# Kernel optimization log

Measured on AMD Instinct MI355X. Metric: run time of the kernel, lower is better.

## Reference

```python
import jax, jax.numpy as jnp
import numpy as np

N, H, S, R, T = 32768, 512, 8, 64, 12

def setup_inputs() -> dict:
    key = jax.random.key(0)
    ks = jax.random.split(key, 7)
    scale = 1.0 / np.sqrt(H)
    return {
        "encodings": jax.random.normal(ks[0], (N, H), dtype=jnp.float32),
        "domain_encs": jax.random.normal(ks[1], (S, H), dtype=jnp.float32),
        "Us": jax.random.normal(ks[2], (S, H, R), dtype=jnp.float32) * scale,
        "W1": jax.random.normal(ks[3], (S, H, H), dtype=jnp.float32) * scale,
        "b1": jax.random.normal(ks[4], (S, H), dtype=jnp.float32) * 0.01,
        "W2": jax.random.normal(ks[5], (S, H, T), dtype=jnp.float32) * scale,
        "b2": jax.random.normal(ks[6], (S, T), dtype=jnp.float32) * 0.01,
    }

def reference(encodings, domain_encs, Us, W1, b1, W2, b2):
    # Mahalanobis soft routing. Original computes (p-mu) @ (U U^T) @ (p-mu)^T
    # and takes sqrt(diag) -- algebraically identical to project-then-square-sum.
    diff = encodings[None, :, :] - domain_encs[:, None, :]        # [S, N, H]
    proj = jnp.einsum('snh,shr->snr', diff, Us)                   # [S, N, R]
    dist = jnp.sqrt(jnp.sum(proj * proj, axis=-1))                # [S, N]
    alphas = jax.nn.softmax(-dist, axis=0)                        # softmax over sources

    # Per-source classifier: Dropout(eval=identity) -> ReLU -> Linear(H,H)
    # -> Dropout -> ReLU -> Linear(H,T) -> Sigmoid
    h0 = jax.nn.relu(encodings)                                   # [N, H]
    h1 = jax.nn.relu(jnp.einsum('nh,shk->snk', h0, W1) + b1[:, None, :])  # [S, N, H]
    out = jax.nn.sigmoid(jnp.einsum('snk,skt->snt', h1, W2) + b2[:, None, :])  # [S, N, T]

    # Softmax-weighted combine of expert outputs
    return jnp.sum(alphas[:, :, None] * out, axis=0)              # [N, T]
```

## Files before the change

### kernel.cpp

```cpp
#include <hip/hip_runtime.h>
#include <hip/hip_bf16.h>

typedef unsigned short u16;
typedef __bf16 bf16x8 __attribute__((ext_vector_type(8)));
typedef float f32x4 __attribute__((ext_vector_type(4)));

#define NROWS 32768
#define H 512
#define NS 8
#define NR 64
#define NT 12

#define WS_W1T   0
#define WS_UCT   4194304
#define WS_W2T   4718592
#define WS_CVEC  4849664
#define WS_ALPH  4851712

union BFU { __bf16 h; u16 u; };
__device__ __forceinline__ u16 f2bf(float v) { BFU b; b.h = (__bf16)v; return b.u; }

__device__ __forceinline__ void gload16(const u16* g, u16* l) {
  __builtin_amdgcn_global_load_lds(
      (const __attribute__((address_space(1))) unsigned int*)g,
      (__attribute__((address_space(3))) unsigned int*)l, 16, 0, 0);
}

__device__ __forceinline__ void stage32(const u16* __restrict__ g, u16* l, int wave, int lane) {
#pragma unroll
  for (int i = 0; i < 8; i++) {
    int r = wave * 8 + i;
    gload16(g + (size_t)r * 512 + (size_t)((lane ^ (r & 7)) * 8), l + r * 512);
  }
}

__global__ __launch_bounds__(256) void transpose_cast(const float* __restrict__ in,
    u16* __restrict__ out, int Rr, int Cc, int Cpad) {
  __shared__ float tile[32][33];
  int b = blockIdx.z, r0 = blockIdx.x * 32, c0 = blockIdx.y * 32;
  int tx = threadIdx.x, ty = threadIdx.y;
#pragma unroll
  for (int i = 0; i < 4; i++) {
    int r = r0 + ty + i * 8, c = c0 + tx;
    float v = 0.f;
    if (r < Rr && c < Cc) v = in[((size_t)b * Rr + r) * Cc + c];
    tile[ty + i * 8][tx] = v;
  }
  __syncthreads();
#pragma unroll
  for (int i = 0; i < 4; i++) {
    int c = c0 + ty + i * 8, r = r0 + tx;
    if (c < Cpad && r < Rr) out[((size_t)b * Cpad + c) * Rr + r] = f2bf(tile[tx][ty + i * 8]);
  }
}

__global__ __launch_bounds__(64) void compute_c(const float* __restrict__ mu,
                                                const float* __restrict__ Us,
                                                float* __restrict__ cvec) {
  int s = blockIdx.x >> 6, r = blockIdx.x & 63, t = threadIdx.x;
  float acc = 0.f;
#pragma unroll
  for (int k = t; k < H; k += 64) acc += mu[s * H + k] * Us[((size_t)s * H + k) * NR + r];
#pragma unroll
  for (int m = 32; m; m >>= 1) acc += __shfl_xor(acc, m, 64);
  if (t == 0) cvec[blockIdx.x] = acc;
}

__global__ __launch_bounds__(256, 2) void routing(
    const float* __restrict__ enc, const u16* __restrict__ UcatT,
    const float* __restrict__ cvec, float* __restrict__ alphT) {
  __shared__ __align__(16) u16 Wst[2][32 * 512];
  __shared__ float distS[NS][64];

  const int tid = threadIdx.x;
  const int wave = tid >> 6, lane = tid & 63;
  const int lnm = lane & 15, lnq = lane >> 4;
  const int row0 = blockIdx.x * 64;

  bf16x8 afrag[16];
  {
    const float* rp = enc + (size_t)(row0 + wave * 16 + lnm) * H + lnq * 8;
#pragma unroll
    for (int ks = 0; ks < 16; ks++) {
      float4 x0 = *(const float4*)(rp + ks * 32);
      float4 x1 = *(const float4*)(rp + ks * 32 + 4);
      bf16x8 a;
      a[0] = (__bf16)x0.x; a[1] = (__bf16)x0.y; a[2] = (__bf16)x0.z; a[3] = (__bf16)x0.w;
      a[4] = (__bf16)x1.x; a[5] = (__bf16)x1.y; a[6] = (__bf16)x1.z; a[7] = (__bf16)x1.w;
      afrag[ks] = a;
    }
  }

  stage32(UcatT, Wst[0], wave, lane);
  float dsq[4] = {0.f, 0.f, 0.f, 0.f};
#pragma unroll 1
  for (int q = 0; q < 16; q++) {
    int s = q >> 1, half = q & 1;
    __syncthreads();
    if (q < 15) stage32(UcatT + (size_t)(q + 1) * 32 * 512, Wst[(q + 1) & 1], wave, lane);
    const u16* buf = Wst[q & 1];
    f32x4 acc[2] = {};
#pragma unroll
    for (int ks = 0; ks < 16; ks++) {
      int uu = ((ks * 4 + lnq) ^ (lnm & 7)) * 8;
      bf16x8 b0 = *(const bf16x8*)&buf[lnm * 512 + uu];
      bf16x8 b1v = *(const bf16x8*)&buf[(16 + lnm) * 512 + uu];
      acc[0] = __builtin_amdgcn_mfma_f32_16x16x32_bf16(afrag[ks], b0, acc[0], 0, 0, 0);
      acc[1] = __builtin_amdgcn_mfma_f32_16x16x32_bf16(afrag[ks], b1v, acc[1], 0, 0, 0);
    }
#pragma unroll
    for (int ct = 0; ct < 2; ct++) {
      float cv = cvec[s * 64 + half * 32 + ct * 16 + lnm];
#pragma unroll
      for (int g = 0; g < 4; g++) { float d = acc[ct][g] - cv; dsq[g] += d * d; }
    }
    if (half == 1) {
#pragma unroll
      for (int m = 1; m < 16; m <<= 1) {
#pragma unroll
        for (int g = 0; g < 4; g++) dsq[g] += __shfl_xor(dsq[g], m, 16);
      }
      if (lnm == 0) {
#pragma unroll
        for (int g = 0; g < 4; g++) distS[s][wave * 16 + lnq * 4 + g] = sqrtf(dsq[g]);
      }
#pragma unroll
      for (int g = 0; g < 4; g++) dsq[g] = 0.f;
    }
  }
  __syncthreads();
  if (tid < 64) {
    float dmin = distS[0][tid];
#pragma unroll
    for (int s = 1; s < NS; s++) dmin = fminf(dmin, distS[s][tid]);
    float den = 0.f, e[NS];
#pragma unroll
    for (int s = 0; s < NS; s++) { e[s] = __expf(dmin - distS[s][tid]); den += e[s]; }
    float inv = 1.f / den;
#pragma unroll
    for (int s = 0; s < NS; s++) alphT[(size_t)s * NROWS + row0 + tid] = e[s] * inv;
  }
}

__global__ __launch_bounds__(256, 2) void moe_main(
    const float* __restrict__ enc, const u16* __restrict__ W1T,
    const u16* __restrict__ W2T, const float* __restrict__ alphT,
    const float* __restrict__ b1g, const float* __restrict__ b2g,
    float* __restrict__ out) {
  __shared__ __align__(16) u16 Wst[2][32 * 512];
  __shared__ __align__(16) u16 h1c[128 * 48];
  __shared__ float alphS[4][128];

  const int tid = threadIdx.x;
  const int wave = tid >> 6, lane = tid & 63;
  const int lnm = lane & 15, lnq = lane >> 4;
  const int rb = blockIdx.x >> 1, sg = blockIdx.x & 1;
  const int row0 = rb * 128, sbase = sg * 4;

#pragma unroll
  for (int i = 0; i < 2; i++) {
    int u = tid + i * 256, j = u >> 7, r = u & 127;
    alphS[j][r] = alphT[(size_t)(sbase + j) * NROWS + row0 + r];
  }

  bf16x8 afrag[2][16];
#pragma unroll
  for (int t = 0; t < 2; t++) {
    const float* rp = enc + (size_t)(row0 + wave * 32 + t * 16 + lnm) * H + lnq * 8;
#pragma unroll
    for (int ks = 0; ks < 16; ks++) {
      float4 x0 = *(const float4*)(rp + ks * 32);
      float4 x1 = *(const float4*)(rp + ks * 32 + 4);
      bf16x8 a;
      a[0] = (__bf16)fmaxf(x0.x, 0.f); a[1] = (__bf16)fmaxf(x0.y, 0.f);
      a[2] = (__bf16)fmaxf(x0.z, 0.f); a[3] = (__bf16)fmaxf(x0.w, 0.f);
      a[4] = (__bf16)fmaxf(x1.x, 0.f); a[5] = (__bf16)fmaxf(x1.y, 0.f);
      a[6] = (__bf16)fmaxf(x1.z, 0.f); a[7] = (__bf16)fmaxf(x1.w, 0.f);
      afrag[t][ks] = a;
    }
  }

  stage32(W1T + (size_t)sbase * 512 * 512, Wst[0], wave, lane);
  f32x4 oacc[2] = {};
  float fin[2][4] = {};
#pragma unroll 1
  for (int q = 0; q < 64; q++) {
    const int j = q >> 4, ch = q & 15;
    const int s = sbase + j;
    __syncthreads();
    if (q < 63) {
      int q1 = q + 1;
      const u16* nb = W1T + ((size_t)(sbase + (q1 >> 4)) * 512 + (q1 & 15) * 32) * 512;
      stage32(nb, Wst[q1 & 1], wave, lane);
    }
    const u16* buf = Wst[q & 1];
    f32x4 acc[2][2] = {};
#pragma unroll
    for (int ks = 0; ks < 16; ks++) {
      int uu = ((ks * 4 + lnq) ^ (lnm & 7)) * 8;
      bf16x8 b0 = *(const bf16x8*)&buf[lnm * 512 + uu];
      bf16x8 b1v = *(const bf16x8*)&buf[(16 + lnm) * 512 + uu];
#pragma unroll
      for (int t = 0; t < 2; t++) {
        acc[t][0] = __builtin_amdgcn_mfma_f32_16x16x32_bf16(afrag[t][ks], b0, acc[t][0], 0, 0, 0);
        acc[t][1] = __builtin_amdgcn_mfma_f32_16x16x32_bf16(afrag[t][ks], b1v, acc[t][1], 0, 0, 0);
      }
    }
    float bb0 = b1g[s * H + ch * 32 + lnm];
    float bb1 = b1g[s * H + ch * 32 + 16 + lnm];
#pragma unroll
    for (int t = 0; t < 2; t++) {
#pragma unroll
      for (int g = 0; g < 4; g++) {
        int rr = wave * 32 + t * 16 + lnq * 4 + g;
        h1c[rr * 48 + lnm]      = f2bf(fmaxf(acc[t][0][g] + bb0, 0.f));
        h1c[rr * 48 + 16 + lnm] = f2bf(fmaxf(acc[t][1][g] + bb1, 0.f));
      }
    }
    bf16x8 bw = *(const bf16x8*)&W2T[((size_t)s * 16 + lnm) * 512 + ch * 32 + lnq * 8];
#pragma unroll
    for (int t = 0; t < 2; t++) {
      bf16x8 a2 = *(const bf16x8*)&h1c[(wave * 32 + t * 16 + lnm) * 48 + lnq * 8];
      oacc[t] = __builtin_amdgcn_mfma_f32_16x16x32_bf16(a2, bw, oacc[t], 0, 0, 0);
    }
    if (ch == 15) {
      float b2v = (lnm < NT) ? b2g[s * NT + lnm] : 0.f;
#pragma unroll
      for (int t = 0; t < 2; t++) {
#pragma unroll
        for (int g = 0; g < 4; g++) {
          float pre = oacc[t][g] + b2v;
          float sig = 1.f / (1.f + __expf(-pre));
          fin[t][g] += alphS[j][wave * 32 + t * 16 + lnq * 4 + g] * sig;
        }
        oacc[t] = (f32x4){0.f, 0.f, 0.f, 0.f};
      }
    }
  }
  if (lnm < NT) {
#pragma unroll
    for (int t = 0; t < 2; t++) {
#pragma unroll
      for (int g = 0; g < 4; g++) {
        int rg = row0 + wave * 32 + t * 16 + lnq * 4 + g;
        atomicAdd(&out[(size_t)rg * NT + lnm], fin[t][g]);
      }
    }
  }
}

extern "C" void kernel_launch(void* const* d_in, const int* in_sizes, int n_in,
                              void* d_out, int out_size, void* d_ws, size_t ws_size,
                              hipStream_t stream) {
  const float* enc = (const float*)d_in[0];
  const float* mu  = (const float*)d_in[1];
  const float* Us  = (const float*)d_in[2];
  const float* W1  = (const float*)d_in[3];
  const float* b1  = (const float*)d_in[4];
  const float* W2  = (const float*)d_in[5];
  const float* b2  = (const float*)d_in[6];
  float* out = (float*)d_out;
  char* ws = (char*)d_ws;
  u16* W1T    = (u16*)(ws + WS_W1T);
  u16* UcatT  = (u16*)(ws + WS_UCT);
  u16* W2T    = (u16*)(ws + WS_W2T);
  float* cvec = (float*)(ws + WS_CVEC);
  float* alphT = (float*)(ws + WS_ALPH);

  dim3 tb(32, 8, 1);
  transpose_cast<<<dim3(16, 16, 8), tb, 0, stream>>>(W1, W1T, 512, 512, 512);
  transpose_cast<<<dim3(16, 2, 8),  tb, 0, stream>>>(Us, UcatT, 512, 64, 64);
  transpose_cast<<<dim3(16, 1, 8),  tb, 0, stream>>>(W2, W2T, 512, 12, 16);
  compute_c<<<512, 64, 0, stream>>>(mu, Us, cvec);
  routing<<<512, 256, 0, stream>>>(enc, UcatT, cvec, alphT);
  hipMemsetAsync(out, 0, (size_t)out_size * sizeof(float), stream);
  moe_main<<<512, 256, 0, stream>>>(enc, W1T, W2T, alphT, b1, b2, out);
}
```

Baseline: 305.8 us.

## Retile moe_main to 256-row blocks with 32x32 MFMA and swapped operands

Rewrites the main MoE kernel so each block handles 256 rows and 2 sources instead of 128 rows and 4 sources. The first GEMM now uses 32x32x16 MFMAs with the weight tile as the A operand and the encodings held in registers as B. W1 chunks are staged in K-halves so the LDS buffers shrink, and occupancy is raised to 3 blocks per CU. The goal is more reuse of each staged weight tile across rows and fewer LDS reads per MFMA. In exchange, register pressure rises (64 bf16x8 fragments per thread) and the h1 tile is written transposed with packed stores.

```diff
diff --git a/kernel.cpp b/kernel.cpp
--- a/kernel.cpp
+++ b/kernel.cpp
@@ -4,6 +4,7 @@
 typedef unsigned short u16;
 typedef __bf16 bf16x8 __attribute__((ext_vector_type(8)));
 typedef float f32x4 __attribute__((ext_vector_type(4)));
+typedef float f32x16 __attribute__((ext_vector_type(16)));
 
 #define NROWS 32768
 #define H 512
@@ -26,14 +27,6 @@
       (__attribute__((address_space(3))) unsigned int*)l, 16, 0, 0);
 }
 
-__device__ __forceinline__ void stage32(const u16* __restrict__ g, u16* l, int wave, int lane) {
-#pragma unroll
-  for (int i = 0; i < 8; i++) {
-    int r = wave * 8 + i;
-    gload16(g + (size_t)r * 512 + (size_t)((lane ^ (r & 7)) * 8), l + r * 512);
-  }
-}
-
 __global__ __launch_bounds__(256) void transpose_cast(const float* __restrict__ in,
     u16* __restrict__ out, int Rr, int Cc, int Cpad) {
   __shared__ float tile[32][33];
@@ -64,6 +57,14 @@
 #pragma unroll
   for (int m = 32; m; m >>= 1) acc += __shfl_xor(acc, m, 64);
   if (t == 0) cvec[blockIdx.x] = acc;
+}
+
+__device__ __forceinline__ void stage32r(const u16* __restrict__ g, u16* l, int wave, int lane) {
+#pragma unroll
+  for (int i = 0; i < 8; i++) {
+    int r = wave * 8 + i;
+    gload16(g + (size_t)r * 512 + (size_t)((lane ^ (r & 7)) * 8), l + r * 512);
+  }
 }
 
 __global__ __launch_bounds__(256, 2) void routing(
@@ -91,13 +92,13 @@
     }
   }
 
-  stage32(UcatT, Wst[0], wave, lane);
+  stage32r(UcatT, Wst[0], wave, lane);
   float dsq[4] = {0.f, 0.f, 0.f, 0.f};
 #pragma unroll 1
   for (int q = 0; q < 16; q++) {
     int s = q >> 1, half = q & 1;
     __syncthreads();
-    if (q < 15) stage32(UcatT + (size_t)(q + 1) * 32 * 512, Wst[(q + 1) & 1], wave, lane);
+    if (q < 15) stage32r(UcatT + (size_t)(q + 1) * 32 * 512, Wst[(q + 1) & 1], wave, lane);
     const u16* buf = Wst[q & 1];
     f32x4 acc[2] = {};
 #pragma unroll
@@ -142,108 +143,142 @@
   }
 }
 
-__global__ __launch_bounds__(256, 2) void moe_main(
+#define H1STR 36
+
+__device__ __forceinline__ void stageW(const u16* __restrict__ g, u16* l, int wave, int lane) {
+  const int half = lane >> 5;
+#pragma unroll
+  for (int i = 0; i < 4; i++) {
+    int rbase = wave * 8 + i * 2;
+    int r = rbase + half;
+    int unit = (lane & 31) ^ (r & 7);
+    gload16(g + (size_t)r * 512 + unit * 8, l + rbase * 256);
+  }
+}
+
+template <int KH>
+__device__ __forceinline__ void gemm1_half(const u16* __restrict__ buf,
+                                           const bf16x8 (&ef)[2][32],
+                                           int lane, f32x16* acc) {
+  const int half = lane >> 5, r31 = lane & 31, rx = r31 & 7;
+  const u16* rowp = buf + r31 * 256;
+#pragma unroll
+  for (int ks = 0; ks < 16; ks++) {
+    bf16x8 a = *(const bf16x8*)&rowp[(((ks * 2 + half) ^ rx) * 8)];
+    acc[0] = __builtin_amdgcn_mfma_f32_32x32x16_bf16(a, ef[0][KH * 16 + ks], acc[0], 0, 0, 0);
+    acc[1] = __builtin_amdgcn_mfma_f32_32x32x16_bf16(a, ef[1][KH * 16 + ks], acc[1], 0, 0, 0);
+  }
+}
+
+__global__ __launch_bounds__(256, 3) void moe_main(
     const float* __restrict__ enc, const u16* __restrict__ W1T,
     const u16* __restrict__ W2T, const float* __restrict__ alphT,
     const float* __restrict__ b1g, const float* __restrict__ b2g,
     float* __restrict__ out) {
-  __shared__ __align__(16) u16 Wst[2][32 * 512];
-  __shared__ __align__(16) u16 h1c[128 * 48];
-  __shared__ float alphS[4][128];
+  __shared__ __align__(16) u16 Wst[2][32 * 256];
+  __shared__ __align__(16) u16 h1c[256 * H1STR];
+  __shared__ float alphS[2][256];
 
   const int tid = threadIdx.x;
   const int wave = tid >> 6, lane = tid & 63;
+  const int half = lane >> 5, l31 = lane & 31;
   const int lnm = lane & 15, lnq = lane >> 4;
-  const int rb = blockIdx.x >> 1, sg = blockIdx.x & 1;
-  const int row0 = rb * 128, sbase = sg * 4;
+  const int rb = blockIdx.x >> 2, sg = blockIdx.x & 3;
+  const int row0 = rb * 256, sbase = sg * 2;
 
 #pragma unroll
   for (int i = 0; i < 2; i++) {
-    int u = tid + i * 256, j = u >> 7, r = u & 127;
+    int u = tid + i * 256, j = u >> 8, r = u & 255;
     alphS[j][r] = alphT[(size_t)(sbase + j) * NROWS + row0 + r];
   }
 
-  bf16x8 afrag[2][16];
-#pragma unroll
-  for (int t = 0; t < 2; t++) {
-    const float* rp = enc + (size_t)(row0 + wave * 32 + t * 16 + lnm) * H + lnq * 8;
-#pragma unroll
-    for (int ks = 0; ks < 16; ks++) {
-      float4 x0 = *(const float4*)(rp + ks * 32);
-      float4 x1 = *(const float4*)(rp + ks * 32 + 4);
+  bf16x8 efrag[2][32];
+#pragma unroll
+  for (int nt = 0; nt < 2; nt++) {
+    const float* rp = enc + (size_t)(row0 + wave * 64 + nt * 32 + l31) * H;
+#pragma unroll
+    for (int ksg = 0; ksg < 32; ksg++) {
+      const float* p = rp + ksg * 16 + half * 8;
+      float4 x0 = *(const float4*)(p);
+      float4 x1 = *(const float4*)(p + 4);
       bf16x8 a;
       a[0] = (__bf16)fmaxf(x0.x, 0.f); a[1] = (__bf16)fmaxf(x0.y, 0.f);
       a[2] = (__bf16)fmaxf(x0.z, 0.f); a[3] = (__bf16)fmaxf(x0.w, 0.f);
       a[4] = (__bf16)fmaxf(x1.x, 0.f); a[5] = (__bf16)fmaxf(x1.y, 0.f);
       a[6] = (__bf16)fmaxf(x1.z, 0.f); a[7] = (__bf16)fmaxf(x1.w, 0.f);
-      afrag[t][ks] = a;
-    }
-  }
-
-  stage32(W1T + (size_t)sbase * 512 * 512, Wst[0], wave, lane);
-  f32x4 oacc[2] = {};
-  float fin[2][4] = {};
+      efrag[nt][ksg] = a;
+    }
+  }
+
+  const f32x16 zero16 = {};
+  f32x16 acc[2];
+  f32x4 oacc[4] = {};
+  float fin[4][4] = {};
+
+  stageW(W1T + (size_t)sbase * 512 * 512, Wst[0], wave, lane);
 #pragma unroll 1
   for (int q = 0; q < 64; q++) {
-    const int j = q >> 4, ch = q & 15;
+    const int j = q >> 5, wc = (q >> 1) & 15, kh = q & 1;
     const int s = sbase + j;
     __syncthreads();
     if (q < 63) {
-      int q1 = q + 1;
-      const u16* nb = W1T + ((size_t)(sbase + (q1 >> 4)) * 512 + (q1 & 15) * 32) * 512;
-      stage32(nb, Wst[q1 & 1], wave, lane);
+      const int t = q + 1;
+      const u16* nb = W1T +
+          ((size_t)((sbase + (t >> 5)) * 512 + ((t >> 1) & 15) * 32)) * 512 + (t & 1) * 256;
+      stageW(nb, Wst[t & 1], wave, lane);
     }
     const u16* buf = Wst[q & 1];
-    f32x4 acc[2][2] = {};
-#pragma unroll
-    for (int ks = 0; ks < 16; ks++) {
-      int uu = ((ks * 4 + lnq) ^ (lnm & 7)) * 8;
-      bf16x8 b0 = *(const bf16x8*)&buf[lnm * 512 + uu];
-      bf16x8 b1v = *(const bf16x8*)&buf[(16 + lnm) * 512 + uu];
-#pragma unroll
-      for (int t = 0; t < 2; t++) {
-        acc[t][0] = __builtin_amdgcn_mfma_f32_16x16x32_bf16(afrag[t][ks], b0, acc[t][0], 0, 0, 0);
-        acc[t][1] = __builtin_amdgcn_mfma_f32_16x16x32_bf16(afrag[t][ks], b1v, acc[t][1], 0, 0, 0);
-      }
-    }
-    float bb0 = b1g[s * H + ch * 32 + lnm];
-    float bb1 = b1g[s * H + ch * 32 + 16 + lnm];
-#pragma unroll
-    for (int t = 0; t < 2; t++) {
+    if (kh == 0) {
+      acc[0] = zero16; acc[1] = zero16;
+      gemm1_half<0>(buf, efrag, lane, acc);
+    } else {
+      gemm1_half<1>(buf, efrag, lane, acc);
+#pragma unroll
+      for (int rq = 0; rq < 4; rq++) {
+        float4 bq = *(const float4*)&b1g[s * H + wc * 32 + 8 * rq + 4 * half];
+#pragma unroll
+        for (int nt = 0; nt < 2; nt++) {
+          int row = wave * 64 + nt * 32 + l31;
+          union { u16 u[4]; uint2 v; } pk;
+          pk.u[0] = f2bf(fmaxf(acc[nt][rq * 4 + 0] + bq.x, 0.f));
+          pk.u[1] = f2bf(fmaxf(acc[nt][rq * 4 + 1] + bq.y, 0.f));
+          pk.u[2] = f2bf(fmaxf(acc[nt][rq * 4 + 2] + bq.z, 0.f));
+          pk.u[3] = f2bf(fmaxf(acc[nt][rq * 4 + 3] + bq.w, 0.f));
+          *(uint2*)&h1c[row * H1STR + 8 * rq + 4 * half] = pk.v;
+        }
+      }
+      bf16x8 bw = *(const bf16x8*)&W2T[((size_t)s * 16 + lnm) * H + wc * 32 + lnq * 8];
+#pragma unroll
+      for (int mt = 0; mt < 4; mt++) {
+        union { uint2 h[2]; bf16x8 v; } a2;
+        const u16* ap = &h1c[(wave * 64 + mt * 16 + lnm) * H1STR + lnq * 8];
+        a2.h[0] = *(const uint2*)(ap);
+        a2.h[1] = *(const uint2*)(ap + 4);
+        oacc[mt] = __builtin_amdgcn_mfma_f32_16x16x32_bf16(a2.v, bw, oacc[mt], 0, 0, 0);
+      }
+      if (wc == 15) {
+        float b2v = (lnm < NT) ? b2g[s * NT + lnm] : 0.f;
+#pragma unroll
+        for (int mt = 0; mt < 4; mt++) {
+          float4 al = *(const float4*)&alphS[j][wave * 64 + mt * 16 + lnq * 4];
+#pragma unroll
+          for (int g = 0; g < 4; g++) {
+            float pre = oacc[mt][g] + b2v;
+            float sig = 1.f / (1.f + __expf(-pre));
+            fin[mt][g] += ((const float*)&al)[g] * sig;
+          }
+          oacc[mt] = (f32x4){0.f, 0.f, 0.f, 0.f};
+        }
+      }
+    }
+  }
+  if (lnm < NT) {
+#pragma unroll
+    for (int mt = 0; mt < 4; mt++) {
 #pragma unroll
       for (int g = 0; g < 4; g++) {
-        int rr = wave * 32 + t * 16 + lnq * 4 + g;
-        h1c[rr * 48 + lnm]      = f2bf(fmaxf(acc[t][0][g] + bb0, 0.f));
-        h1c[rr * 48 + 16 + lnm] = f2bf(fmaxf(acc[t][1][g] + bb1, 0.f));
-      }
-    }
-    bf16x8 bw = *(const bf16x8*)&W2T[((size_t)s * 16 + lnm) * 512 + ch * 32 + lnq * 8];
-#pragma unroll
-    for (int t = 0; t < 2; t++) {
-      bf16x8 a2 = *(const bf16x8*)&h1c[(wave * 32 + t * 16 + lnm) * 48 + lnq * 8];
-      oacc[t] = __builtin_amdgcn_mfma_f32_16x16x32_bf16(a2, bw, oacc[t], 0, 0, 0);
-    }
-    if (ch == 15) {
-      float b2v = (lnm < NT) ? b2g[s * NT + lnm] : 0.f;
-#pragma unroll
-      for (int t = 0; t < 2; t++) {
-#pragma unroll
-        for (int g = 0; g < 4; g++) {
-          float pre = oacc[t][g] + b2v;
-          float sig = 1.f / (1.f + __expf(-pre));
-          fin[t][g] += alphS[j][wave * 32 + t * 16 + lnq * 4 + g] * sig;
-        }
-        oacc[t] = (f32x4){0.f, 0.f, 0.f, 0.f};
-      }
-    }
-  }
-  if (lnm < NT) {
-#pragma unroll
-    for (int t = 0; t < 2; t++) {
-#pragma unroll
-      for (int g = 0; g < 4; g++) {
-        int rg = row0 + wave * 32 + t * 16 + lnq * 4 + g;
-        atomicAdd(&out[(size_t)rg * NT + lnm], fin[t][g]);
+        int rg = row0 + wave * 64 + mt * 16 + lnq * 4 + g;
+        atomicAdd(&out[(size_t)rg * NT + lnm], fin[mt][g]);
       }
     }
   }
```

After: 950.0 us. +210.6%, slower.

## Split moe_main over 2-source groups with half-K weight stages for occupancy

Applied to the files above, without the earlier changes.

The MoE kernel now splits sources into four groups of two, giving 1024 blocks, and stages W1 in half-K chunks (32x256). This halves the LDS weight buffers and allows 3 blocks per CU. The MFMA operand order is swapped so accumulators map rows to lanes and h1 can be stored as packed 8-byte writes with a narrower stride. Output is accumulated with an atomic per source instead of one per block, and each weight chunk now takes twice as many barrier iterations.

```diff
diff --git a/kernel.cpp b/kernel.cpp
--- a/kernel.cpp
+++ b/kernel.cpp
@@ -26,14 +26,6 @@
       (__attribute__((address_space(3))) unsigned int*)l, 16, 0, 0);
 }
 
-__device__ __forceinline__ void stage32(const u16* __restrict__ g, u16* l, int wave, int lane) {
-#pragma unroll
-  for (int i = 0; i < 8; i++) {
-    int r = wave * 8 + i;
-    gload16(g + (size_t)r * 512 + (size_t)((lane ^ (r & 7)) * 8), l + r * 512);
-  }
-}
-
 __global__ __launch_bounds__(256) void transpose_cast(const float* __restrict__ in,
     u16* __restrict__ out, int Rr, int Cc, int Cpad) {
   __shared__ float tile[32][33];
@@ -64,6 +56,14 @@
 #pragma unroll
   for (int m = 32; m; m >>= 1) acc += __shfl_xor(acc, m, 64);
   if (t == 0) cvec[blockIdx.x] = acc;
+}
+
+__device__ __forceinline__ void stage32r(const u16* __restrict__ g, u16* l, int wave, int lane) {
+#pragma unroll
+  for (int i = 0; i < 8; i++) {
+    int r = wave * 8 + i;
+    gload16(g + (size_t)r * 512 + (size_t)((lane ^ (r & 7)) * 8), l + r * 512);
+  }
 }
 
 __global__ __launch_bounds__(256, 2) void routing(
@@ -91,13 +91,13 @@
     }
   }
 
-  stage32(UcatT, Wst[0], wave, lane);
+  stage32r(UcatT, Wst[0], wave, lane);
   float dsq[4] = {0.f, 0.f, 0.f, 0.f};
 #pragma unroll 1
   for (int q = 0; q < 16; q++) {
     int s = q >> 1, half = q & 1;
     __syncthreads();
-    if (q < 15) stage32(UcatT + (size_t)(q + 1) * 32 * 512, Wst[(q + 1) & 1], wave, lane);
+    if (q < 15) stage32r(UcatT + (size_t)(q + 1) * 32 * 512, Wst[(q + 1) & 1], wave, lane);
     const u16* buf = Wst[q & 1];
     f32x4 acc[2] = {};
 #pragma unroll
@@ -142,28 +142,36 @@
   }
 }
 
-__global__ __launch_bounds__(256, 2) void moe_main(
+#define H1STR 40
+
+__device__ __forceinline__ void stageW16(const u16* __restrict__ g, u16* l, int tid) {
+#pragma unroll
+  for (int i = 0; i < 4; i++) {
+    int flat = tid + i * 256;
+    int r = flat >> 5, u = flat & 31;
+    gload16(g + (size_t)r * 512 + (u ^ (r & 7)) * 8, l + flat * 8);
+  }
+}
+
+__global__ __launch_bounds__(256, 3) void moe_main(
     const float* __restrict__ enc, const u16* __restrict__ W1T,
     const u16* __restrict__ W2T, const float* __restrict__ alphT,
     const float* __restrict__ b1g, const float* __restrict__ b2g,
     float* __restrict__ out) {
-  __shared__ __align__(16) u16 Wst[2][32 * 512];
-  __shared__ __align__(16) u16 h1c[128 * 48];
-  __shared__ float alphS[4][128];
+  __shared__ __align__(16) u16 Wst[2][32 * 256];
+  __shared__ __align__(16) u16 h1c[128 * H1STR];
+  __shared__ float alphS[2][128];
 
   const int tid = threadIdx.x;
   const int wave = tid >> 6, lane = tid & 63;
   const int lnm = lane & 15, lnq = lane >> 4;
-  const int rb = blockIdx.x >> 1, sg = blockIdx.x & 1;
-  const int row0 = rb * 128, sbase = sg * 4;
-
-#pragma unroll
-  for (int i = 0; i < 2; i++) {
-    int u = tid + i * 256, j = u >> 7, r = u & 127;
-    alphS[j][r] = alphT[(size_t)(sbase + j) * NROWS + row0 + r];
-  }
-
-  bf16x8 afrag[2][16];
+  const int rb = blockIdx.x & 255, sg = blockIdx.x >> 8;
+  const int row0 = rb * 128, sbase = sg * 2;
+
+  { int j = tid >> 7, r = tid & 127;
+    alphS[j][r] = alphT[(size_t)(sbase + j) * NROWS + row0 + r]; }
+
+  bf16x8 efrag[2][16];
 #pragma unroll
   for (int t = 0; t < 2; t++) {
     const float* rp = enc + (size_t)(row0 + wave * 32 + t * 16 + lnm) * H + lnq * 8;
@@ -176,74 +184,75 @@
       a[2] = (__bf16)fmaxf(x0.z, 0.f); a[3] = (__bf16)fmaxf(x0.w, 0.f);
       a[4] = (__bf16)fmaxf(x1.x, 0.f); a[5] = (__bf16)fmaxf(x1.y, 0.f);
       a[6] = (__bf16)fmaxf(x1.z, 0.f); a[7] = (__bf16)fmaxf(x1.w, 0.f);
-      afrag[t][ks] = a;
-    }
-  }
-
-  stage32(W1T + (size_t)sbase * 512 * 512, Wst[0], wave, lane);
+      efrag[t][ks] = a;
+    }
+  }
+
+  stageW16(W1T + (size_t)sbase * 512 * 512, Wst[0], tid);
+  f32x4 acc[2][2];
   f32x4 oacc[2] = {};
-  float fin[2][4] = {};
 #pragma unroll 1
   for (int q = 0; q < 64; q++) {
-    const int j = q >> 4, ch = q & 15;
+    const int j = q >> 5, ch = (q >> 1) & 15, kh = q & 1;
     const int s = sbase + j;
     __syncthreads();
     if (q < 63) {
-      int q1 = q + 1;
-      const u16* nb = W1T + ((size_t)(sbase + (q1 >> 4)) * 512 + (q1 & 15) * 32) * 512;
-      stage32(nb, Wst[q1 & 1], wave, lane);
+      const int t = q + 1;
+      const u16* nb = W1T +
+          ((size_t)((sbase + (t >> 5)) * 512 + ((t >> 1) & 15) * 32)) * 512 + (t & 1) * 256;
+      stageW16(nb, Wst[t & 1], tid);
     }
     const u16* buf = Wst[q & 1];
-    f32x4 acc[2][2] = {};
-#pragma unroll
-    for (int ks = 0; ks < 16; ks++) {
-      int uu = ((ks * 4 + lnq) ^ (lnm & 7)) * 8;
-      bf16x8 b0 = *(const bf16x8*)&buf[lnm * 512 + uu];
-      bf16x8 b1v = *(const bf16x8*)&buf[(16 + lnm) * 512 + uu];
+    if (kh == 0) {
+#pragma unroll
+      for (int t = 0; t < 2; t++) { acc[t][0] = (f32x4){0,0,0,0}; acc[t][1] = (f32x4){0,0,0,0}; }
+    }
+#pragma unroll
+    for (int ks = 0; ks < 8; ks++) {
+      const int uu = ((ks * 4 + lnq) ^ (lnm & 7)) * 8;
+      bf16x8 w0 = *(const bf16x8*)&buf[lnm * 256 + uu];
+      bf16x8 w1 = *(const bf16x8*)&buf[(16 + lnm) * 256 + uu];
 #pragma unroll
       for (int t = 0; t < 2; t++) {
-        acc[t][0] = __builtin_amdgcn_mfma_f32_16x16x32_bf16(afrag[t][ks], b0, acc[t][0], 0, 0, 0);
-        acc[t][1] = __builtin_amdgcn_mfma_f32_16x16x32_bf16(afrag[t][ks], b1v, acc[t][1], 0, 0, 0);
-      }
-    }
-    float bb0 = b1g[s * H + ch * 32 + lnm];
-    float bb1 = b1g[s * H + ch * 32 + 16 + lnm];
-#pragma unroll
-    for (int t = 0; t < 2; t++) {
-#pragma unroll
-      for (int g = 0; g < 4; g++) {
-        int rr = wave * 32 + t * 16 + lnq * 4 + g;
-        h1c[rr * 48 + lnm]      = f2bf(fmaxf(acc[t][0][g] + bb0, 0.f));
-        h1c[rr * 48 + 16 + lnm] = f2bf(fmaxf(acc[t][1][g] + bb1, 0.f));
-      }
-    }
-    bf16x8 bw = *(const bf16x8*)&W2T[((size_t)s * 16 + lnm) * 512 + ch * 32 + lnq * 8];
-#pragma unroll
-    for (int t = 0; t < 2; t++) {
-      bf16x8 a2 = *(const bf16x8*)&h1c[(wave * 32 + t * 16 + lnm) * 48 + lnq * 8];
-      oacc[t] = __builtin_amdgcn_mfma_f32_16x16x32_bf16(a2, bw, oacc[t], 0, 0, 0);
-    }
-    if (ch == 15) {
-      float b2v = (lnm < NT) ? b2g[s * NT + lnm] : 0.f;
+        acc[t][0] = __builtin_amdgcn_mfma_f32_16x16x32_bf16(w0, efrag[t][kh * 8 + ks], acc[t][0], 0, 0, 0);
+        acc[t][1] = __builtin_amdgcn_mfma_f32_16x16x32_bf16(w1, efrag[t][kh * 8 + ks], acc[t][1], 0, 0, 0);
+      }
+    }
+    if (kh == 1) {
+#pragma unroll
+      for (int ct = 0; ct < 2; ct++) {
+        float4 bq = *(const float4*)&b1g[s * H + ch * 32 + ct * 16 + lnq * 4];
+#pragma unroll
+        for (int t = 0; t < 2; t++) {
+          union { u16 u[4]; uint2 v; } pk;
+          pk.u[0] = f2bf(fmaxf(acc[t][ct][0] + bq.x, 0.f));
+          pk.u[1] = f2bf(fmaxf(acc[t][ct][1] + bq.y, 0.f));
+          pk.u[2] = f2bf(fmaxf(acc[t][ct][2] + bq.z, 0.f));
+          pk.u[3] = f2bf(fmaxf(acc[t][ct][3] + bq.w, 0.f));
+          *(uint2*)&h1c[(wave * 32 + t * 16 + lnm) * H1STR + ct * 16 + lnq * 4] = pk.v;
+        }
+      }
+      bf16x8 bw = *(const bf16x8*)&W2T[((size_t)s * 16 + lnm) * H + ch * 32 + lnq * 8];
 #pragma unroll
       for (int t = 0; t < 2; t++) {
-#pragma unroll
-        for (int g = 0; g < 4; g++) {
-          float pre = oacc[t][g] + b2v;
-          float sig = 1.f / (1.f + __expf(-pre));
-          fin[t][g] += alphS[j][wave * 32 + t * 16 + lnq * 4 + g] * sig;
+        bf16x8 a2 = *(const bf16x8*)&h1c[(wave * 32 + t * 16 + lnm) * H1STR + lnq * 8];
+        oacc[t] = __builtin_amdgcn_mfma_f32_16x16x32_bf16(a2, bw, oacc[t], 0, 0, 0);
+      }
+      if (ch == 15) {
+        float b2v = (lnm < NT) ? b2g[s * NT + lnm] : 0.f;
+#pragma unroll
+        for (int t = 0; t < 2; t++) {
+#pragma unroll
+          for (int g = 0; g < 4; g++) {
+            float sig = 1.f / (1.f + __expf(-(oacc[t][g] + b2v)));
+            float av = alphS[j][wave * 32 + t * 16 + lnq * 4 + g];
+            if (lnm < NT) {
+              int rg = row0 + wave * 32 + t * 16 + lnq * 4 + g;
+              atomicAdd(&out[(size_t)rg * NT + lnm], av * sig);
+            }
+          }
+          oacc[t] = (f32x4){0.f, 0.f, 0.f, 0.f};
         }
-        oacc[t] = (f32x4){0.f, 0.f, 0.f, 0.f};
-      }
-    }
-  }
-  if (lnm < NT) {
-#pragma unroll
-    for (int t = 0; t < 2; t++) {
-#pragma unroll
-      for (int g = 0; g < 4; g++) {
-        int rg = row0 + wave * 32 + t * 16 + lnq * 4 + g;
-        atomicAdd(&out[(size_t)rg * NT + lnm], fin[t][g]);
       }
     }
   }
@@ -274,5 +283,5 @@
   compute_c<<<512, 64, 0, stream>>>(mu, Us, cvec);
   routing<<<512, 256, 0, stream>>>(enc, UcatT, cvec, alphT);
   hipMemsetAsync(out, 0, (size_t)out_size * sizeof(float), stream);
-  moe_main<<<512, 256, 0, stream>>>(enc, W1T, W2T, alphT, b1, b2, out);
-}
+  moe_main<<<1024, 256, 0, stream>>>(enc, W1T, W2T, alphT, b1, b2, out);
+}
```

After: 882.0 us. 2.88x slower.
